# Kernel optimization log

Hardware: AMD Instinct MI355X
Metric: run time of the kernel (lower is better)

The kernel has to match this reference:

```python
import jax, jax.numpy as jnp
import numpy as np

TWO_PI = 2.0 * np.pi


def quat2mat3(q):
    # q: (B,4) (w,x,y,z), normalized internally -> (B,3,3)
    q = q / jnp.linalg.norm(q, axis=-1, keepdims=True)
    w, x, y, z = q[:, 0], q[:, 1], q[:, 2], q[:, 3]
    R = jnp.stack([
        1 - 2 * (y * y + z * z), 2 * (x * y - w * z), 2 * (x * z + w * y),
        2 * (x * y + w * z), 1 - 2 * (x * x + z * z), 2 * (y * z - w * x),
        2 * (x * z - w * y), 2 * (y * z + w * x), 1 - 2 * (x * x + y * y),
    ], axis=-1).reshape(-1, 3, 3)
    return R


def se3(R, t):
    # R: (B,3,3), t: (B,3) -> (B,4,4)
    B = R.shape[0]
    top = jnp.concatenate([R, t[:, :, None]], axis=2)            # (B,3,4)
    bottom = jnp.broadcast_to(jnp.array([[0., 0., 0., 1.]], R.dtype), (B, 1, 4))
    return jnp.concatenate([top, bottom], axis=1)


def mat2quat(R):
    # batched rotation matrix -> quaternion (w,x,y,z), branchless 4-case Shepperd
    R00, R01, R02 = R[:, 0, 0], R[:, 0, 1], R[:, 0, 2]
    R10, R11, R12 = R[:, 1, 0], R[:, 1, 1], R[:, 1, 2]
    R20, R21, R22 = R[:, 2, 0], R[:, 2, 1], R[:, 2, 2]
    tr = R00 + R11 + R22
    t0 = 1.0 + tr
    t1 = 1.0 + R00 - R11 - R22
    t2 = 1.0 - R00 + R11 - R22
    t3 = 1.0 - R00 - R11 + R22
    q0 = jnp.stack([t0, R21 - R12, R02 - R20, R10 - R01], axis=-1)
    q1 = jnp.stack([R21 - R12, t1, R01 + R10, R02 + R20], axis=-1)
    q2 = jnp.stack([R02 - R20, R01 + R10, t2, R12 + R21], axis=-1)
    q3 = jnp.stack([R10 - R01, R02 + R20, R12 + R21, t3], axis=-1)
    qs = jnp.stack([q0, q1, q2, q3], axis=1)   # (B,4,4)
    ts = jnp.stack([t0, t1, t2, t3], axis=1)   # (B,4)
    diag = jnp.stack([R00, R11, R22], axis=1)
    sel = jnp.where(tr > 0, 0, 1 + jnp.argmax(diag, axis=1))
    q = jnp.take_along_axis(qs, sel[:, None, None].astype(jnp.int32).repeat(4, 2), axis=1)[:, 0]
    t = jnp.take_along_axis(ts, sel[:, None].astype(jnp.int32), axis=1)[:, 0]
    return q * (0.5 / jnp.sqrt(jnp.clip(t, 1e-12)))[:, None]


def quat_mul(a, b):
    aw, av = a[:, :1], a[:, 1:]
    bw, bv = b[:, :1], b[:, 1:]
    w = aw * bw - jnp.sum(av * bv, axis=1, keepdims=True)
    v = aw * bv + bw * av + jnp.cross(av, bv)
    return jnp.concatenate([w, v], axis=1)


def quat_distance(q, r):
    r_inv = jnp.concatenate([r[:, :1], -r[:, 1:]], axis=1)  # conjugate (unit quats)
    d = quat_mul(q, r_inv)
    return 2.0 * jnp.arctan2(jnp.linalg.norm(d[:, 1:], axis=1), jnp.abs(d[:, 0]))


def smooth_l1(x, y):
    d = jnp.abs(x - y)
    return jnp.where(d < 1.0, 0.5 * d * d, d - 0.5)


def _rand_se3(key, B):
    kq, kt = jax.random.split(key)
    q = jax.random.normal(kq, (B, 4), jnp.float32)
    R = quat2mat3(q)
    t = jax.random.normal(kt, (B, 3), jnp.float32)
    return se3(R, t)


def setup_inputs() -> dict:
    key = jax.random.key(0)
    B, N = 8, 1_000_000
    k1, k2, k3, k4, k5 = jax.random.split(key, 5)
    return {
        "pred_translation": 0.1 * jax.random.normal(k1, (B, 3), jnp.float32),
        "pred_rotation": jax.random.normal(k2, (B, 4), jnp.float32),
        "pcs": 20.0 * jax.random.normal(k3, (B, N, 3), jnp.float32),
        "gt_T_to_camera": _rand_se3(k4, B),
        "init_T_to_camera": _rand_se3(k5, B),
        "mask": jnp.ones((B, N), jnp.int32),
    }


def reference(pred_translation, pred_rotation, pcs, gt_T_to_camera, init_T_to_camera, mask):
    W_T, W_R, W_PC, W_QN = 1.0, 0.5, 0.5, 0.5
    B = pcs.shape[0]

    # quat norm loss on raw predicted quaternion
    norm_sq = jnp.sum(pred_rotation ** 2, axis=1)
    qn_loss = jnp.mean((norm_sq - 1.0) ** 2)

    # T_pred = trans(t) @ rot(q)  -> (B,4,4)
    T_t = se3(jnp.broadcast_to(jnp.eye(3, dtype=pcs.dtype), (B, 3, 3)), pred_translation)
    T_r = se3(quat2mat3(pred_rotation), jnp.zeros((B, 3), pcs.dtype))
    T_pred = jnp.einsum('bij,bjk->bik', T_t, T_r)

    # T_gt_expected = inv(T_pred) @ init_T
    T_gt_exp = jnp.einsum('bij,bjk->bik', jnp.linalg.inv(T_pred), init_T_to_camera)
    p_t = T_gt_exp[:, :3, 3]
    p_R = T_gt_exp[:, :3, :3]
    g_t = gt_T_to_camera[:, :3, 3]
    g_R = gt_T_to_camera[:, :3, :3]

    # translation: smooth-L1, sum over axes, mean over batch
    t_loss = jnp.mean(jnp.sum(smooth_l1(p_t, g_t), axis=1))

    # PC reprojection: RT_total = inv(gt_T) @ [p_R|p_t]
    T_pred2 = se3(p_R, p_t)
    RT = jnp.einsum('bij,bjk->bik', jnp.linalg.inv(gt_T_to_camera), T_pred2)
    pts = jnp.einsum('bij,bnj->bni', RT[:, :3, :3], pcs) + RT[:, None, :3, 3]
    err = jnp.linalg.norm(pts - pcs, axis=2)               # (B,N)
    mf = mask.astype(pcs.dtype)
    pc_loss = jnp.mean(jnp.sum(err * mf, axis=1) / jnp.sum(mf, axis=1))

    # rotation: quaternion geodesic distance between matrix-derived quats
    r_loss = jnp.mean(quat_distance(mat2quat(p_R), mat2quat(g_R)))

    loss = W_T * t_loss + W_R * r_loss + W_PC * pc_loss + W_QN * qn_loss
    return loss
```

## Files before the change

### kernel.cpp

```cpp
#include <hip/hip_runtime.h>
#include <math.h>

struct Pose {
    float M[9], Tt[3], pR[9], pt[3], gR[9], gt[3], qn;
};

__device__ __forceinline__ float smooth_l1f(float x, float y) {
    float d = fabsf(x - y);
    return d < 1.0f ? 0.5f * d * d : d - 0.5f;
}

__device__ void mat2quat_dev(const float* R, float* q) {
    float R00=R[0],R01=R[1],R02=R[2];
    float R10=R[3],R11=R[4],R12=R[5];
    float R20=R[6],R21=R[7],R22=R[8];
    float tr = R00 + R11 + R22;
    float t;
    if (tr > 0.0f) {
        t = 1.0f + tr;
        q[0]=t; q[1]=R21-R12; q[2]=R02-R20; q[3]=R10-R01;
    } else {
        int sel = 1; float best = R00;
        if (R11 > best) { sel = 2; best = R11; }
        if (R22 > best) { sel = 3; }
        if (sel == 1)      { t = 1.0f+R00-R11-R22; q[0]=R21-R12; q[1]=t; q[2]=R01+R10; q[3]=R02+R20; }
        else if (sel == 2) { t = 1.0f-R00+R11-R22; q[0]=R02-R20; q[1]=R01+R10; q[2]=t; q[3]=R12+R21; }
        else               { t = 1.0f-R00-R11+R22; q[0]=R10-R01; q[1]=R02+R20; q[2]=R12+R21; q[3]=t; }
    }
    float s = 0.5f / sqrtf(fmaxf(t, 1e-12f));
    q[0]*=s; q[1]*=s; q[2]*=s; q[3]*=s;
}

__device__ void compute_pose(int b,
                             const float* __restrict__ pred_t,
                             const float* __restrict__ pred_q,
                             const float* __restrict__ gtT,
                             const float* __restrict__ initT,
                             Pose& P)
{
    float tx=pred_t[b*3+0], ty=pred_t[b*3+1], tz=pred_t[b*3+2];
    float q0=pred_q[b*4+0], q1=pred_q[b*4+1], q2=pred_q[b*4+2], q3=pred_q[b*4+3];
    float nsq = q0*q0+q1*q1+q2*q2+q3*q3;
    P.qn = (nsq-1.0f)*(nsq-1.0f);
    float inv = rsqrtf(nsq);
    float w=q0*inv, x=q1*inv, y=q2*inv, z=q3*inv;
    float R[9];
    R[0]=1.0f-2.0f*(y*y+z*z); R[1]=2.0f*(x*y-w*z);      R[2]=2.0f*(x*z+w*y);
    R[3]=2.0f*(x*y+w*z);      R[4]=1.0f-2.0f*(x*x+z*z); R[5]=2.0f*(y*z-w*x);
    R[6]=2.0f*(x*z-w*y);      R[7]=2.0f*(y*z+w*x);      R[8]=1.0f-2.0f*(x*x+y*y);

    float iR[9], it[3];
    for (int i=0;i<3;i++){
        for (int j=0;j<3;j++){
            iR[i*3+j]=initT[b*16+i*4+j];
            P.gR[i*3+j]=gtT[b*16+i*4+j];
        }
        it[i]=initT[b*16+i*4+3];
        P.gt[i]=gtT[b*16+i*4+3];
    }
    for (int i=0;i<3;i++){
        for (int j=0;j<3;j++)
            P.pR[i*3+j] = R[0+i]*iR[0+j] + R[3+i]*iR[3+j] + R[6+i]*iR[6+j];
        P.pt[i] = R[0+i]*(it[0]-tx) + R[3+i]*(it[1]-ty) + R[6+i]*(it[2]-tz);
    }
    for (int i=0;i<3;i++){
        for (int j=0;j<3;j++)
            P.M[i*3+j] = P.gR[0+i]*P.pR[0+j] + P.gR[3+i]*P.pR[3+j] + P.gR[6+i]*P.pR[6+j];
        P.Tt[i] = P.gR[0+i]*(P.pt[0]-P.gt[0]) + P.gR[3+i]*(P.pt[1]-P.gt[1]) + P.gR[6+i]*(P.pt[2]-P.gt[2]);
    }
    P.M[0]-=1.0f; P.M[4]-=1.0f; P.M[8]-=1.0f;
}

#define TP  1024
#define F4T 768

__global__ __launch_bounds__(256) void pc_fused(const float* __restrict__ pcs,
                                                const int* __restrict__ mask,
                                                const float* __restrict__ pred_t,
                                                const float* __restrict__ pred_q,
                                                const float* __restrict__ gtT,
                                                const float* __restrict__ initT,
                                                float* __restrict__ errS,
                                                float* __restrict__ maskS,
                                                int N, int bpb, int chunk)
{
    int b   = blockIdx.x / bpb;
    int blk = blockIdx.x - b*bpb;
    int t   = threadIdx.x;

    __shared__ float sMT[12];
    __shared__ float sP[2][F4T*4];
    __shared__ float sE[4], sM[4];

    int r0 = blk * chunk;
    if (r0 >= N) {
        if (t==0){ errS[blockIdx.x]=0.0f; maskS[blockIdx.x]=0.0f; }
        return;
    }
    int my_pts = N - r0; if (my_pts > chunk) my_pts = chunk;
    int nt    = (my_pts + TP - 1) / TP;
    int my_f4 = (my_pts * 3) >> 2;
    int my_m4 = my_pts >> 2;

    const float4* pf4 = (const float4*)pcs  + ((size_t)b*N + r0)*3/4;
    const int4*   mi4 = (const int4*)  mask + ((size_t)b*N + r0)/4;

    if (t == 0) {
        Pose P;
        compute_pose(b, pred_t, pred_q, gtT, initT, P);
        #pragma unroll
        for (int k=0;k<9;k++) sMT[k]=P.M[k];
        sMT[9]=P.Tt[0]; sMT[10]=P.Tt[1]; sMT[11]=P.Tt[2];
    }

    float4 rA = make_float4(0,0,0,0);
    float4 rB = make_float4(0,0,0,0);
    float4 rC = make_float4(0,0,0,0);
    int4   rM = make_int4(0,0,0,0);

    auto stage = [&](int ti) {
        int fb = ti * F4T;
        if (ti*TP + TP <= my_pts) {
            rA = pf4[fb       + t];
            rB = pf4[fb + 256 + t];
            rC = pf4[fb + 512 + t];
            rM = mi4[ti*256 + t];
        } else {
            int s0 = fb + t, s1 = fb + 256 + t, s2 = fb + 512 + t, sm = ti*256 + t;
            rA = (s0 < my_f4) ? pf4[s0] : make_float4(0,0,0,0);
            rB = (s1 < my_f4) ? pf4[s1] : make_float4(0,0,0,0);
            rC = (s2 < my_f4) ? pf4[s2] : make_float4(0,0,0,0);
            rM = (sm < my_m4) ? mi4[sm] : make_int4(0,0,0,0);
        }
    };
    auto wr = [&](int buf) {
        float4* d = (float4*)sP[buf];
        d[t      ] = rA;
        d[t + 256] = rB;
        d[t + 512] = rC;
    };

    stage(0);
    __syncthreads();
    float m00=sMT[0], m01=sMT[1], m02=sMT[2];
    float m10=sMT[3], m11=sMT[4], m12=sMT[5];
    float m20=sMT[6], m21=sMT[7], m22=sMT[8];
    float t0 =sMT[9], t1 =sMT[10], t2 =sMT[11];
    wr(0);
    __syncthreads();

    float esum = 0.0f, msum = 0.0f;
    for (int ti = 0; ti < nt; ti++) {
        int cur = ti & 1;
        int4 cM = rM;
        if (ti + 1 < nt) stage(ti + 1);

        const float4* sp4 = (const float4*)sP[cur];
        float4 A = sp4[3*t], C = sp4[3*t+1], D = sp4[3*t+2];
        float px[4] = {A.x, A.w, C.z, D.y};
        float py[4] = {A.y, C.x, C.w, D.z};
        float pz[4] = {A.z, C.y, D.x, D.w};
        float mf[4] = {(float)cM.x, (float)cM.y, (float)cM.z, (float)cM.w};
        #pragma unroll
        for (int j=0;j<4;j++){
            float dx = fmaf(m00,px[j], fmaf(m01,py[j], fmaf(m02,pz[j], t0)));
            float dy = fmaf(m10,px[j], fmaf(m11,py[j], fmaf(m12,pz[j], t1)));
            float dz = fmaf(m20,px[j], fmaf(m21,py[j], fmaf(m22,pz[j], t2)));
            esum = fmaf(mf[j], sqrtf(fmaf(dx,dx, fmaf(dy,dy, dz*dz))), esum);
            msum += mf[j];
        }

        if (ti + 1 < nt) wr(cur ^ 1);
        __syncthreads();
    }

    for (int off=32; off>0; off>>=1){
        esum += __shfl_down(esum, off);
        msum += __shfl_down(msum, off);
    }
    int lane = t & 63, wid = t >> 6;
    if (lane==0){ sE[wid]=esum; sM[wid]=msum; }
    __syncthreads();
    if (t==0){
        errS [blockIdx.x] = sE[0]+sE[1]+sE[2]+sE[3];
        maskS[blockIdx.x] = sM[0]+sM[1]+sM[2]+sM[3];
    }
}

__global__ void finish_kernel(const float* __restrict__ errS,
                              const float* __restrict__ maskS,
                              const float* __restrict__ pred_t,
                              const float* __restrict__ pred_q,
                              const float* __restrict__ gtT,
                              const float* __restrict__ initT,
                              float* __restrict__ out, int B, int bpb)
{
    int t = threadIdx.x, lane = t & 63, w = t >> 6;
    __shared__ double sPC[4];
    double acc = 0.0;
    for (int b = w; b < B; b += 4) {
        float e=0.0f, m=0.0f;
        for (int k=lane; k<bpb; k+=64){ e += errS[b*bpb+k]; m += maskS[b*bpb+k]; }
        for (int off=32; off>0; off>>=1){
            e += __shfl_down(e, off);
            m += __shfl_down(m, off);
        }
        if (lane==0) acc += (double)e / (double)m;
    }
    if (lane==0) sPC[w] = acc;

    float partial = 0.0f;
    if (t < B) {
        Pose P;
        compute_pose(t, pred_t, pred_q, gtT, initT, P);
        float t_term = smooth_l1f(P.pt[0],P.gt[0]) + smooth_l1f(P.pt[1],P.gt[1])
                     + smooth_l1f(P.pt[2],P.gt[2]);
        float qp[4], qg[4];
        mat2quat_dev(P.pR,qp); mat2quat_dev(P.gR,qg);
        float dw  = qp[0]*qg[0] + qp[1]*qg[1] + qp[2]*qg[2] + qp[3]*qg[3];
        float cx  = qp[2]*qg[3]-qp[3]*qg[2];
        float cy  = qp[3]*qg[1]-qp[1]*qg[3];
        float cz  = qp[1]*qg[2]-qp[2]*qg[1];
        float dvx = -qp[0]*qg[1] + qg[0]*qp[1] - cx;
        float dvy = -qp[0]*qg[2] + qg[0]*qp[2] - cy;
        float dvz = -qp[0]*qg[3] + qg[0]*qp[3] - cz;
        float r_term = 2.0f*atan2f(sqrtf(dvx*dvx+dvy*dvy+dvz*dvz), fabsf(dw));
        partial = (1.0f*t_term + 0.5f*r_term + 0.5f*P.qn) / (float)B;
    }
    if (w==0)
        for (int off=32; off>0; off>>=1) partial += __shfl_down(partial, off);
    __syncthreads();
    if (t==0){
        double pc = sPC[0]+sPC[1]+sPC[2]+sPC[3];
        out[0] = partial + 0.5f * (float)(pc / (double)B);
    }
}

extern "C" void kernel_launch(void* const* d_in, const int* in_sizes, int n_in,
                              void* d_out, int out_size, void* d_ws, size_t ws_size,
                              hipStream_t stream)
{
    const float* pred_t = (const float*)d_in[0];
    const float* pred_q = (const float*)d_in[1];
    const float* pcs    = (const float*)d_in[2];
    const float* gtT    = (const float*)d_in[3];
    const float* initT  = (const float*)d_in[4];
    const int*   mask   = (const int*)d_in[5];

    int B = in_sizes[0] / 3;
    int N = in_sizes[2] / (B * 3);

    int bpb   = 192;
    int chunk = (((N + bpb - 1) / bpb) + 3) & ~3;

    float* errS  = (float*)d_ws;
    float* maskS = errS + B*bpb;
    float* out   = (float*)d_out;

    pc_fused<<<B*bpb, 256, 0, stream>>>(pcs, mask, pred_t, pred_q, gtT, initT,
                                        errS, maskS, N, bpb, chunk);
    finish_kernel<<<1, 256, 0, stream>>>(errS, maskS, pred_t, pred_q, gtT, initT,
                                         out, B, bpb);
}
```

Baseline: 31.36 us.

## Fuse finish reduction into main kernel via last-block atomic counter

Merges the separate finish kernel into the point-cloud kernel. The last block to finish is detected with an atomic counter and performs the final per-batch reduction and loss computation. Pose computation now overlaps with the first tile load. This removes one kernel launch and its inter-kernel gap, but adds a memset launch, atomics and a fence, and assumes B*32 <= 256 threads for the final reduction.

```diff
diff --git a/kernel.cpp b/kernel.cpp
--- a/kernel.cpp
+++ b/kernel.cpp
@@ -74,104 +74,106 @@
 #define TP  1024
 #define F4T 768
 
-__global__ __launch_bounds__(256) void pc_fused(const float* __restrict__ pcs,
-                                                const int* __restrict__ mask,
-                                                const float* __restrict__ pred_t,
-                                                const float* __restrict__ pred_q,
-                                                const float* __restrict__ gtT,
-                                                const float* __restrict__ initT,
-                                                float* __restrict__ errS,
-                                                float* __restrict__ maskS,
-                                                int N, int bpb, int chunk)
+__global__ __launch_bounds__(256) void pc_all(const float* __restrict__ pcs,
+                                              const int* __restrict__ mask,
+                                              const float* __restrict__ pred_t,
+                                              const float* __restrict__ pred_q,
+                                              const float* __restrict__ gtT,
+                                              const float* __restrict__ initT,
+                                              unsigned* __restrict__ counter,
+                                              float* __restrict__ errS,
+                                              float* __restrict__ maskS,
+                                              float* __restrict__ out,
+                                              int N, int bpb, int chunk, int B)
 {
-    int b   = blockIdx.x / bpb;
-    int blk = blockIdx.x - b*bpb;
+    int bid = blockIdx.x;
+    int b   = bid / bpb;
+    int blk = bid - b*bpb;
     int t   = threadIdx.x;
 
     __shared__ float sMT[12];
     __shared__ float sP[2][F4T*4];
     __shared__ float sE[4], sM[4];
-
+    __shared__ int   sLast;
+
+    float esum = 0.0f, msum = 0.0f;
     int r0 = blk * chunk;
-    if (r0 >= N) {
-        if (t==0){ errS[blockIdx.x]=0.0f; maskS[blockIdx.x]=0.0f; }
-        return;
-    }
-    int my_pts = N - r0; if (my_pts > chunk) my_pts = chunk;
-    int nt    = (my_pts + TP - 1) / TP;
-    int my_f4 = (my_pts * 3) >> 2;
-    int my_m4 = my_pts >> 2;
-
-    const float4* pf4 = (const float4*)pcs  + ((size_t)b*N + r0)*3/4;
-    const int4*   mi4 = (const int4*)  mask + ((size_t)b*N + r0)/4;
-
-    if (t == 0) {
-        Pose P;
-        compute_pose(b, pred_t, pred_q, gtT, initT, P);
-        #pragma unroll
-        for (int k=0;k<9;k++) sMT[k]=P.M[k];
-        sMT[9]=P.Tt[0]; sMT[10]=P.Tt[1]; sMT[11]=P.Tt[2];
-    }
-
-    float4 rA = make_float4(0,0,0,0);
-    float4 rB = make_float4(0,0,0,0);
-    float4 rC = make_float4(0,0,0,0);
-    int4   rM = make_int4(0,0,0,0);
-
-    auto stage = [&](int ti) {
-        int fb = ti * F4T;
-        if (ti*TP + TP <= my_pts) {
-            rA = pf4[fb       + t];
-            rB = pf4[fb + 256 + t];
-            rC = pf4[fb + 512 + t];
-            rM = mi4[ti*256 + t];
-        } else {
-            int s0 = fb + t, s1 = fb + 256 + t, s2 = fb + 512 + t, sm = ti*256 + t;
-            rA = (s0 < my_f4) ? pf4[s0] : make_float4(0,0,0,0);
-            rB = (s1 < my_f4) ? pf4[s1] : make_float4(0,0,0,0);
-            rC = (s2 < my_f4) ? pf4[s2] : make_float4(0,0,0,0);
-            rM = (sm < my_m4) ? mi4[sm] : make_int4(0,0,0,0);
-        }
-    };
-    auto wr = [&](int buf) {
-        float4* d = (float4*)sP[buf];
-        d[t      ] = rA;
-        d[t + 256] = rB;
-        d[t + 512] = rC;
-    };
-
-    stage(0);
-    __syncthreads();
-    float m00=sMT[0], m01=sMT[1], m02=sMT[2];
-    float m10=sMT[3], m11=sMT[4], m12=sMT[5];
-    float m20=sMT[6], m21=sMT[7], m22=sMT[8];
-    float t0 =sMT[9], t1 =sMT[10], t2 =sMT[11];
-    wr(0);
-    __syncthreads();
-
-    float esum = 0.0f, msum = 0.0f;
-    for (int ti = 0; ti < nt; ti++) {
-        int cur = ti & 1;
-        int4 cM = rM;
-        if (ti + 1 < nt) stage(ti + 1);
-
-        const float4* sp4 = (const float4*)sP[cur];
-        float4 A = sp4[3*t], C = sp4[3*t+1], D = sp4[3*t+2];
-        float px[4] = {A.x, A.w, C.z, D.y};
-        float py[4] = {A.y, C.x, C.w, D.z};
-        float pz[4] = {A.z, C.y, D.x, D.w};
-        float mf[4] = {(float)cM.x, (float)cM.y, (float)cM.z, (float)cM.w};
-        #pragma unroll
-        for (int j=0;j<4;j++){
-            float dx = fmaf(m00,px[j], fmaf(m01,py[j], fmaf(m02,pz[j], t0)));
-            float dy = fmaf(m10,px[j], fmaf(m11,py[j], fmaf(m12,pz[j], t1)));
-            float dz = fmaf(m20,px[j], fmaf(m21,py[j], fmaf(m22,pz[j], t2)));
-            esum = fmaf(mf[j], sqrtf(fmaf(dx,dx, fmaf(dy,dy, dz*dz))), esum);
-            msum += mf[j];
-        }
-
-        if (ti + 1 < nt) wr(cur ^ 1);
+
+    if (r0 < N) {
+        int my_pts = N - r0; if (my_pts > chunk) my_pts = chunk;
+        int nt    = (my_pts + TP - 1) / TP;
+        int my_f4 = (my_pts * 3) >> 2;
+        int my_m4 = my_pts >> 2;
+
+        const float4* pf4 = (const float4*)pcs  + ((size_t)b*N + r0)*3/4;
+        const int4*   mi4 = (const int4*)  mask + ((size_t)b*N + r0)/4;
+
+        float4 rA = make_float4(0,0,0,0);
+        float4 rB = make_float4(0,0,0,0);
+        float4 rC = make_float4(0,0,0,0);
+        int4   rM = make_int4(0,0,0,0);
+
+        auto stage = [&](int ti) {
+            int fb = ti * F4T;
+            if (ti*TP + TP <= my_pts) {
+                rA = pf4[fb       + t];
+                rB = pf4[fb + 256 + t];
+                rC = pf4[fb + 512 + t];
+                rM = mi4[ti*256 + t];
+            } else {
+                int s0 = fb + t, s1 = fb + 256 + t, s2 = fb + 512 + t, sm = ti*256 + t;
+                rA = (s0 < my_f4) ? pf4[s0] : make_float4(0,0,0,0);
+                rB = (s1 < my_f4) ? pf4[s1] : make_float4(0,0,0,0);
+                rC = (s2 < my_f4) ? pf4[s2] : make_float4(0,0,0,0);
+                rM = (sm < my_m4) ? mi4[sm] : make_int4(0,0,0,0);
+            }
+        };
+        auto wr = [&](int buf) {
+            float4* d = (float4*)sP[buf];
+            d[t      ] = rA;
+            d[t + 256] = rB;
+            d[t + 512] = rC;
+        };
+
+        stage(0);
+        if (t == 0) {
+            Pose P;
+            compute_pose(b, pred_t, pred_q, gtT, initT, P);
+            #pragma unroll
+            for (int k=0;k<9;k++) sMT[k]=P.M[k];
+            sMT[9]=P.Tt[0]; sMT[10]=P.Tt[1]; sMT[11]=P.Tt[2];
+        }
         __syncthreads();
+        float m00=sMT[0], m01=sMT[1], m02=sMT[2];
+        float m10=sMT[3], m11=sMT[4], m12=sMT[5];
+        float m20=sMT[6], m21=sMT[7], m22=sMT[8];
+        float t0 =sMT[9], t1 =sMT[10], t2 =sMT[11];
+        wr(0);
+        __syncthreads();
+
+        for (int ti = 0; ti < nt; ti++) {
+            int cur = ti & 1;
+            int4 cM = rM;
+            if (ti + 1 < nt) stage(ti + 1);
+
+            const float4* sp4 = (const float4*)sP[cur];
+            float4 A = sp4[3*t], C = sp4[3*t+1], D = sp4[3*t+2];
+            float px[4] = {A.x, A.w, C.z, D.y};
+            float py[4] = {A.y, C.x, C.w, D.z};
+            float pz[4] = {A.z, C.y, D.x, D.w};
+            float mf[4] = {(float)cM.x, (float)cM.y, (float)cM.z, (float)cM.w};
+            #pragma unroll
+            for (int j=0;j<4;j++){
+                float dx = fmaf(m00,px[j], fmaf(m01,py[j], fmaf(m02,pz[j], t0)));
+                float dy = fmaf(m10,px[j], fmaf(m11,py[j], fmaf(m12,pz[j], t1)));
+                float dz = fmaf(m20,px[j], fmaf(m21,py[j], fmaf(m22,pz[j], t2)));
+                esum = fmaf(mf[j], sqrtf(fmaf(dx,dx, fmaf(dy,dy, dz*dz))), esum);
+                msum += mf[j];
+            }
+
+            if (ti + 1 < nt) wr(cur ^ 1);
+            __syncthreads();
+        }
     }
 
     for (int off=32; off>0; off>>=1){
@@ -182,35 +184,32 @@
     if (lane==0){ sE[wid]=esum; sM[wid]=msum; }
     __syncthreads();
     if (t==0){
-        errS [blockIdx.x] = sE[0]+sE[1]+sE[2]+sE[3];
-        maskS[blockIdx.x] = sM[0]+sM[1]+sM[2]+sM[3];
-    }
-}
-
-__global__ void finish_kernel(const float* __restrict__ errS,
-                              const float* __restrict__ maskS,
-                              const float* __restrict__ pred_t,
-                              const float* __restrict__ pred_q,
-                              const float* __restrict__ gtT,
-                              const float* __restrict__ initT,
-                              float* __restrict__ out, int B, int bpb)
-{
-    int t = threadIdx.x, lane = t & 63, w = t >> 6;
-    __shared__ double sPC[4];
-    double acc = 0.0;
-    for (int b = w; b < B; b += 4) {
-        float e=0.0f, m=0.0f;
-        for (int k=lane; k<bpb; k+=64){ e += errS[b*bpb+k]; m += maskS[b*bpb+k]; }
-        for (int off=32; off>0; off>>=1){
-            e += __shfl_down(e, off);
-            m += __shfl_down(m, off);
-        }
-        if (lane==0) acc += (double)e / (double)m;
-    }
-    if (lane==0) sPC[w] = acc;
+        atomicExch(&errS [bid], sE[0]+sE[1]+sE[2]+sE[3]);
+        atomicExch(&maskS[bid], sM[0]+sM[1]+sM[2]+sM[3]);
+        __threadfence();
+        unsigned old = atomicAdd(counter, 1u);
+        sLast = (old == (unsigned)(gridDim.x - 1)) ? 1 : 0;
+    }
+    __syncthreads();
+    if (!sLast) return;
+
+    int g = t >> 5, sub = t & 31;
+    double e = 0.0, m = 0.0;
+    if (g < B) {
+        for (int k = sub; k < bpb; k += 32) {
+            e += (double)atomicAdd(&errS [g*bpb + k], 0.0f);
+            m += (double)atomicAdd(&maskS[g*bpb + k], 0.0f);
+        }
+    }
+    double* dE = (double*)&sP[0][0];
+    double* dM = dE + 256;
+    dE[t] = e; dM[t] = m;
+    __syncthreads();
 
     float partial = 0.0f;
     if (t < B) {
+        double te = 0.0, tm = 0.0;
+        for (int j = 0; j < 32; j++){ te += dE[t*32 + j]; tm += dM[t*32 + j]; }
         Pose P;
         compute_pose(t, pred_t, pred_q, gtT, initT, P);
         float t_term = smooth_l1f(P.pt[0],P.gt[0]) + smooth_l1f(P.pt[1],P.gt[1])
@@ -225,14 +224,12 @@
         float dvy = -qp[0]*qg[2] + qg[0]*qp[2] - cy;
         float dvz = -qp[0]*qg[3] + qg[0]*qp[3] - cz;
         float r_term = 2.0f*atan2f(sqrtf(dvx*dvx+dvy*dvy+dvz*dvz), fabsf(dw));
-        partial = (1.0f*t_term + 0.5f*r_term + 0.5f*P.qn) / (float)B;
-    }
-    if (w==0)
+        partial = (1.0f*t_term + 0.5f*r_term + 0.5f*P.qn) / (float)B
+                + (float)(0.5 * (te / tm) / (double)B);
+    }
+    if (t < 64) {
         for (int off=32; off>0; off>>=1) partial += __shfl_down(partial, off);
-    __syncthreads();
-    if (t==0){
-        double pc = sPC[0]+sPC[1]+sPC[2]+sPC[3];
-        out[0] = partial + 0.5f * (float)(pc / (double)B);
+        if (t==0) out[0] = partial;
     }
 }
 
@@ -252,13 +249,14 @@
 
     int bpb   = 192;
     int chunk = (((N + bpb - 1) / bpb) + 3) & ~3;
-
-    float* errS  = (float*)d_ws;
-    float* maskS = errS + B*bpb;
-    float* out   = (float*)d_out;
-
-    pc_fused<<<B*bpb, 256, 0, stream>>>(pcs, mask, pred_t, pred_q, gtT, initT,
-                                        errS, maskS, N, bpb, chunk);
-    finish_kernel<<<1, 256, 0, stream>>>(errS, maskS, pred_t, pred_q, gtT, initT,
-                                         out, B, bpb);
-}
+    int grid  = B * bpb;
+
+    unsigned* counter = (unsigned*)d_ws;
+    float*    errS    = (float*)d_ws + 64;
+    float*    maskS   = errS + grid;
+    float*    out     = (float*)d_out;
+
+    hipMemsetAsync(counter, 0, sizeof(unsigned), stream);
+    pc_all<<<grid, 256, 0, stream>>>(pcs, mask, pred_t, pred_q, gtT, initT,
+                                     counter, errS, maskS, out, N, bpb, chunk, B);
+}
```

Result: slower. 67.32 us (+114.6%).
